# Kernel tuning notes

Hardware: AMD Instinct MI355X
Metric: run time of the kernel (lower is better)

## Reference

```python
import jax, jax.numpy as jnp
import numpy as np

N = 50000   # nodes
E = 800000  # edges
G = 64      # graphs in batch
H1, D1 = 2, 64   # gat1: 2 heads x 64
D2 = 32          # gat2: 1 head x 32
IN = 1
EPS = 1e-5


def _gat(h, src, dst, W, al, ar, Wres, bias, Hh, D):
    # DGL GATConv (eval mode): project, per-edge attention, edge softmax over dst, scatter-sum, residual + bias
    feat = (h @ W).reshape(N, Hh, D)                     # [N,H,D]
    el = jnp.sum(feat * al, axis=-1)                     # [N,H]
    er = jnp.sum(feat * ar, axis=-1)                     # [N,H]
    e = jax.nn.leaky_relu(el[src] + er[dst], 0.2)        # [E,H]
    m = jax.ops.segment_max(e, dst, num_segments=N)      # [N,H] (stable softmax)
    a = jnp.exp(e - m[dst])
    s = jax.ops.segment_sum(a, dst, num_segments=N)
    alpha = a / s[dst]                                   # [E,H]
    msg = feat[src] * alpha[:, :, None]                  # [E,H,D]
    rst = jax.ops.segment_sum(msg, dst, num_segments=N)  # [N,H,D]
    res = (h @ Wres).reshape(N, Hh, D)
    return rst + res + bias.reshape(1, Hh, D)


def _bn(x, gamma, beta, mean, var):
    return (x - mean) * jax.lax.rsqrt(var + EPS) * gamma + beta


def setup_inputs() -> dict:
    key = jax.random.key(0)
    ks = jax.random.split(key, 32)
    rn = lambda i, shape: jax.random.normal(ks[i], shape, jnp.float32) * 0.1
    inp = {
        'feat': jax.random.normal(ks[0], (N, IN), jnp.float32),
        'W1': rn(1, (IN, H1 * D1)), 'al1': rn(2, (H1, D1)), 'ar1': rn(3, (H1, D1)),
        'res1': rn(4, (IN, H1 * D1)), 'b1': rn(5, (H1 * D1,)),
        'g1_gamma': jnp.ones((H1 * D1,), jnp.float32), 'g1_beta': jnp.zeros((H1 * D1,), jnp.float32),
        'g1_mean': rn(6, (H1 * D1,)), 'g1_var': jax.random.uniform(ks[7], (H1 * D1,), jnp.float32) + 0.5,
        'W2': rn(8, (H1 * D1, D2)), 'al2': rn(9, (1, D2)), 'ar2': rn(10, (1, D2)),
        'res2': rn(11, (H1 * D1, D2)), 'b2': rn(12, (D2,)),
        'g2_gamma': jnp.ones((D2,), jnp.float32), 'g2_beta': jnp.zeros((D2,), jnp.float32),
        'g2_mean': rn(13, (D2,)), 'g2_var': jax.random.uniform(ks[14], (D2,), jnp.float32) + 0.5,
        'Wd1': rn(15, (D2, H1 * D1)), 'bd1': rn(16, (H1 * D1,)),
        'gd_gamma': jnp.ones((H1 * D1,), jnp.float32), 'gd_beta': jnp.zeros((H1 * D1,), jnp.float32),
        'gd_mean': rn(17, (H1 * D1,)), 'gd_var': jax.random.uniform(ks[18], (H1 * D1,), jnp.float32) + 0.5,
        'Wd2': rn(19, (H1 * D1, IN)), 'bd2': rn(20, (IN,)),
        'src': jax.random.randint(ks[21], (E,), 0, N, jnp.int32),
        'dst': jax.random.randint(ks[22], (E,), 0, N, jnp.int32),
        'graph_ids': jnp.sort(jax.random.randint(ks[23], (N,), 0, G, jnp.int32)),
    }
    return inp


def reference(feat, W1, al1, ar1, res1, b1, g1_gamma, g1_beta, g1_mean, g1_var,
              W2, al2, ar2, res2, b2, g2_gamma, g2_beta, g2_mean, g2_var,
              Wd1, bd1, gd_gamma, gd_beta, gd_mean, gd_var, Wd2, bd2,
              src, dst, graph_ids):
    h = _gat(feat, src, dst, W1, al1, ar1, res1, b1, H1, D1)   # [N,2,64]
    h = h.reshape(N, H1 * D1)
    h = jax.nn.relu(_bn(h, g1_gamma, g1_beta, g1_mean, g1_var))
    h = _gat(h, src, dst, W2, al2, ar2, res2, b2, 1, D2)       # [N,1,32]
    h = h.reshape(N, D2)
    h = jax.nn.relu(_bn(h, g2_gamma, g2_beta, g2_mean, g2_var))
    # dgl.mean_nodes over batched graphs
    counts = jax.ops.segment_sum(jnp.ones((N,), h.dtype), graph_ids, num_segments=G)
    graph_rep = jax.ops.segment_sum(h, graph_ids, num_segments=G) / jnp.maximum(counts, 1.0)[:, None]
    # decoder: Linear -> BN -> ReLU -> Linear (dropout off in eval)
    d = jax.nn.relu(_bn(h @ Wd1 + bd1, gd_gamma, gd_beta, gd_mean, gd_var))
    reconstruction = d @ Wd2 + bd2
    return graph_rep, reconstruction
```

## Files before the change

### kernel.cpp

```cpp
#include <hip/hip_runtime.h>
#include <hip/hip_bf16.h>

#define NN 50000
#define NE 800000
#define NG 64
#define C1 128
#define D2 32
#define CAP 32
#define BN_EPS 1e-5f

#define CST_A   0
#define CST_B   2
#define CST_P   4
#define CST_Q   132
#define CST_R   260
#define CST_SC2 388
#define CST_RC2 420
#define CST_SD  452
#define CST_RD  580
#define CST_N   1024

#define UO_DEG   0
#define UO_OVFC  50000
#define ZERO_UNITS 50004
#define UO_FLAG  50004
#define UO_CST   50008
#define UO_ESRC2 51040
#define UO_OVF   851040
#define UO_FCAN  2451040
#define UO_F2    2501040
#define UO_RS2   3301040
#define UO_EL2   4901040
#define UO_ER2   4951040
#define UO_END   5001040

__device__ __forceinline__ float lrelu(float x) { return fmaxf(x, 0.2f * x); }
__device__ __forceinline__ float bu2f(unsigned int u) {
    union { unsigned int i; float f; } v; v.i = (u & 0xFFFFu) << 16; return v.f;
}
__device__ __forceinline__ unsigned short f2bu(float f) {
    union { float f; unsigned int i; } v; v.f = f;
    unsigned int r = v.i + 0x7FFFu + ((v.i >> 16) & 1u);
    return (unsigned short)(r >> 16);
}
__device__ __forceinline__ float pk_lo(unsigned int w) {
    union { unsigned int i; float f; } v; v.i = w << 16; return v.f;
}
__device__ __forceinline__ float pk_hi(unsigned int w) {
    union { unsigned int i; float f; } v; v.i = w & 0xFFFF0000u; return v.f;
}
__device__ __forceinline__ float ldw(const void* p, int i, int bf) {
    return bf ? bu2f(((const unsigned short*)p)[i]) : ((const float*)p)[i];
}
__device__ __forceinline__ int sniff64(const unsigned int* fw, int l) {
    int cnt = 0;
    for (int j = l; j < 256; j += 64) {
        unsigned int b = (fw[j] >> 8) & 0x7Fu;
        cnt += (b >= 0x3Au && b <= 0x41u) ? 1 : 0;
    }
#pragma unroll
    for (int m = 32; m >= 1; m >>= 1) cnt += __shfl_xor(cnt, m);
    return (cnt > 128) ? 1 : 0;
}

__global__ void k_prep(const void* __restrict__ feat, const int* __restrict__ dst,
                       const int* __restrict__ src,
                       float* __restrict__ fcan, int* __restrict__ deg,
                       unsigned short* __restrict__ esrc2,
                       int2* __restrict__ ovf, int* __restrict__ ovfc,
                       const void* W1, const void* al1, const void* ar1,
                       const void* res1, const void* b1,
                       const void* g1g, const void* g1b, const void* g1m, const void* g1v,
                       const void* b2v, const void* g2g, const void* g2b,
                       const void* g2m, const void* g2v,
                       const void* bd1, const void* gdg, const void* gdb,
                       const void* gdm, const void* gdv,
                       int* __restrict__ flag, float* __restrict__ cst) {
    __shared__ int sBf;
    int t = threadIdx.x;
    if (t < 64) {
        int bf = sniff64((const unsigned int*)feat, t);
        if (t == 0) sBf = bf;
    }
    __syncthreads();
    int bf = sBf;

    if (blockIdx.x == 0) {
        if (t == 0) *flag = bf;
        if (t < 128) {
            if (t < 2) {
                float a = 0.0f, b = 0.0f;
                for (int d = 0; d < 64; ++d) {
                    float w = ldw(W1, t * 64 + d, bf);
                    a += w * ldw(al1, t * 64 + d, bf);
                    b += w * ldw(ar1, t * 64 + d, bf);
                }
                cst[CST_A + t] = a;
                cst[CST_B + t] = b;
            }
            {
                float sc = rsqrtf(ldw(g1v, t, bf) + BN_EPS) * ldw(g1g, t, bf);
                cst[CST_P + t] = ldw(W1, t, bf) * sc;
                cst[CST_Q + t] = ldw(res1, t, bf) * sc;
                cst[CST_R + t] = (ldw(b1, t, bf) - ldw(g1m, t, bf)) * sc + ldw(g1b, t, bf);
            }
            if (t < D2) {
                float sc = rsqrtf(ldw(g2v, t, bf) + BN_EPS) * ldw(g2g, t, bf);
                cst[CST_SC2 + t] = sc;
                cst[CST_RC2 + t] = (ldw(b2v, t, bf) - ldw(g2m, t, bf)) * sc + ldw(g2b, t, bf);
            }
            {
                float sc = rsqrtf(ldw(gdv, t, bf) + BN_EPS) * ldw(gdg, t, bf);
                cst[CST_SD + t] = sc;
                cst[CST_RD + t] = (ldw(bd1, t, bf) - ldw(gdm, t, bf)) * sc + ldw(gdb, t, bf);
            }
        }
    }

    int k = blockIdx.x * blockDim.x + t;
    if (k < NN) fcan[k] = ldw(feat, k, bf);
    if (k < NE) {
        int d = dst[k];
        int slot = atomicAdd(&deg[d], 1);
        if (slot < CAP) {
            esrc2[d * CAP + slot] = (unsigned short)src[k];
        } else {
            int p = atomicAdd(ovfc, 1);
            ovf[p] = make_int2(d, src[k]);
        }
    }
}

__global__ __launch_bounds__(256) void k_layer1(
        const float* __restrict__ fcan, const void* W2, const void* res2,
        const void* al2, const void* ar2,
        const int* __restrict__ flag, const float* __restrict__ cst,
        const int* __restrict__ deg, const unsigned short* __restrict__ esrc2,
        const int2* __restrict__ ovf, const int* __restrict__ ovfc,
        unsigned short* __restrict__ F2, float* __restrict__ RS2,
        float* __restrict__ EL2, float* __restrict__ ER2) {
    __shared__ unsigned int sW2pk[32 * 66];
    __shared__ unsigned int sR2pk[32 * 66];
    __shared__ unsigned int sH1pk[32 * 66];
    __shared__ float sP[C1], sQ[C1], sR[C1];
    __shared__ float sAl[D2], sAr[D2];
    int t = threadIdx.x;
    int bf = *flag;
    for (int u = t; u < 2048; u += 256) {
        int cw = u >> 5, l2 = u & 31;
        unsigned int wlo = (unsigned int)f2bu(ldw(W2, cw * D2 + l2, bf));
        unsigned int whi = (unsigned int)f2bu(ldw(W2, (cw + 64) * D2 + l2, bf));
        sW2pk[l2 * 66 + cw] = wlo | (whi << 16);
        unsigned int rlo = (unsigned int)f2bu(ldw(res2, cw * D2 + l2, bf));
        unsigned int rhi = (unsigned int)f2bu(ldw(res2, (cw + 64) * D2 + l2, bf));
        sR2pk[l2 * 66 + cw] = rlo | (rhi << 16);
    }
    if (t < C1) { sP[t] = cst[CST_P + t]; sQ[t] = cst[CST_Q + t]; sR[t] = cst[CST_R + t]; }
    if (t < D2) { sAl[t] = ldw(al2, t, bf); sAr[t] = ldw(ar2, t, bf); }
    __syncthreads();

    int l = t & 31;
    int g = t >> 5;
    int base = blockIdx.x * 32;
    float A0 = cst[CST_A + 0], A1 = cst[CST_A + 1];
    float B0 = cst[CST_B + 0], B1 = cst[CST_B + 1];

    int dcap[4], draw[4];
    float fiK[4];
#pragma unroll
    for (int k = 0; k < 4; ++k) {
        int i = base + g * 4 + k;
        if (i < NN) {
            draw[k] = deg[i];
            dcap[k] = draw[k] < CAP ? draw[k] : CAP;
            fiK[k] = fcan[i];
        } else { draw[k] = 0; dcap[k] = 0; fiK[k] = 0.0f; }
    }
    float S0[4], S1[4], N0[4], N1[4];
#pragma unroll
    for (int k = 0; k < 4; ++k) { S0[k] = S1[k] = N0[k] = N1[k] = 0.0f; }
    int sA[4];
#pragma unroll
    for (int k = 0; k < 4; ++k)
        sA[k] = (l < dcap[k]) ? (int)esrc2[(base + g * 4 + k) * CAP + l] : 0;
    float fA[4];
#pragma unroll
    for (int k = 0; k < 4; ++k) fA[k] = fcan[sA[k]];
#pragma unroll
    for (int k = 0; k < 4; ++k) {
        if (l < dcap[k]) {
            float w0 = __expf(lrelu(A0 * fA[k] + B0 * fiK[k]));
            float w1 = __expf(lrelu(A1 * fA[k] + B1 * fiK[k]));
            S0[k] += w0; N0[k] += w0 * fA[k];
            S1[k] += w1; N1[k] += w1 * fA[k];
        }
    }
#pragma unroll
    for (int k = 0; k < 4; ++k) {
        if (draw[k] > CAP) {
            int i = base + g * 4 + k;
            int novf = *ovfc;
            for (int p = l; p < novf; p += 32) {
                int2 o = ovf[p];
                if (o.x == i) {
                    float fs = fcan[o.y];
                    float w0 = __expf(lrelu(A0 * fs + B0 * fiK[k]));
                    float w1 = __expf(lrelu(A1 * fs + B1 * fiK[k]));
                    S0[k] += w0; N0[k] += w0 * fs;
                    S1[k] += w1; N1[k] += w1 * fs;
                }
            }
        }
    }
#pragma unroll
    for (int m = 16; m >= 1; m >>= 1) {
#pragma unroll
        for (int k = 0; k < 4; ++k) {
            S0[k] += __shfl_xor(S0[k], m); N0[k] += __shfl_xor(N0[k], m);
            S1[k] += __shfl_xor(S1[k], m); N1[k] += __shfl_xor(N1[k], m);
        }
    }
#pragma unroll
    for (int k = 0; k < 4; ++k) {
        int slot = g * 4 + k;
        float T0 = S0[k] > 0.0f ? N0[k] / S0[k] : 0.0f;
        float T1 = S1[k] > 0.0f ? N1[k] / S1[k] : 0.0f;
        float h0  = fmaxf(sP[l]      * T0 + sQ[l]      * fiK[k] + sR[l],      0.0f);
        float h1v = fmaxf(sP[l + 32] * T0 + sQ[l + 32] * fiK[k] + sR[l + 32], 0.0f);
        float h2v = fmaxf(sP[l + 64] * T1 + sQ[l + 64] * fiK[k] + sR[l + 64], 0.0f);
        float h3v = fmaxf(sP[l + 96] * T1 + sQ[l + 96] * fiK[k] + sR[l + 96], 0.0f);
        sH1pk[slot * 66 + l]      = (unsigned int)f2bu(h0)  | ((unsigned int)f2bu(h2v) << 16);
        sH1pk[slot * 66 + l + 32] = (unsigned int)f2bu(h1v) | ((unsigned int)f2bu(h3v) << 16);
    }
    __syncthreads();

    int w = t >> 6;
    int half = (t >> 5) & 1;
    int nb0 = w * 8 + half * 4;
    float aF[4] = {0.f, 0.f, 0.f, 0.f}, aR[4] = {0.f, 0.f, 0.f, 0.f};
    for (int cw = 0; cw < 64; cw += 2) {
        uint2 wq = *(const uint2*)&sW2pk[l * 66 + cw];
        uint2 rq = *(const uint2*)&sR2pk[l * 66 + cw];
        float w_a = pk_lo(wq.x), w_b = pk_hi(wq.x), w_c = pk_lo(wq.y), w_d = pk_hi(wq.y);
        float r_a = pk_lo(rq.x), r_b = pk_hi(rq.x), r_c = pk_lo(rq.y), r_d = pk_hi(rq.y);
#pragma unroll
        for (int n = 0; n < 4; ++n) {
            uint2 hq = *(const uint2*)&sH1pk[(nb0 + n) * 66 + cw];
            float h_a = pk_lo(hq.x), h_b = pk_hi(hq.x), h_c = pk_lo(hq.y), h_d = pk_hi(hq.y);
            aF[n] = fmaf(h_a, w_a, fmaf(h_b, w_b, fmaf(h_c, w_c, fmaf(h_d, w_d, aF[n]))));
            aR[n] = fmaf(h_a, r_a, fmaf(h_b, r_b, fmaf(h_c, r_c, fmaf(h_d, r_d, aR[n]))));
        }
    }
#pragma unroll
    for (int n = 0; n < 4; ++n) {
        int i = base + nb0 + n;
        if (i < NN) {
            float elp = aF[n] * sAl[l], erp = aF[n] * sAr[l];
#pragma unroll
            for (int m = 16; m >= 1; m >>= 1) {
                elp += __shfl_xor(elp, m);
                erp += __shfl_xor(erp, m);
            }
            if (l == 0) { EL2[i] = elp; ER2[i] = erp; }
            F2[(size_t)i * D2 + l]  = f2bu(aF[n]);
            RS2[(size_t)i * D2 + l] = aR[n];
        }
    }
}

__global__ __launch_bounds__(256) void k_final(
        const void* Wd1, const void* Wd2, const void* bd2,
        const int* __restrict__ flag, const float* __restrict__ cst,
        const int* __restrict__ deg, const unsigned short* __restrict__ esrc2,
        const int2* __restrict__ ovf, const int* __restrict__ ovfc,
        const unsigned short* __restrict__ F2, float* __restrict__ RS2,
        const float* __restrict__ EL2, const float* __restrict__ ER2,
        float* __restrict__ out) {
    __shared__ float sWd1[C1 * D2];
    __shared__ float sWd2[C1];
    __shared__ float sSd[C1], sRd[C1];
    __shared__ float sSc2[D2], sRc2[D2];
    __shared__ float sH2[8 * D2];
    int t = threadIdx.x;
    int bf = *flag;
    for (int u = t; u < C1 * D2; u += 256) sWd1[u] = ldw(Wd1, u, bf);
    for (int u = t; u < C1; u += 256) {
        sWd2[u] = ldw(Wd2, u, bf);
        sSd[u] = cst[CST_SD + u]; sRd[u] = cst[CST_RD + u];
    }
    if (t < D2) { sSc2[t] = cst[CST_SC2 + t]; sRc2[t] = cst[CST_RC2 + t]; }
    __syncthreads();

    int i = (blockIdx.x * 256 + t) >> 5;
    int l = t & 31;
    int nb = t >> 5;

    float eri = ER2[i];
    int dr = deg[i];
    int dcap = dr < CAP ? dr : CAP;
    const unsigned short* row = &esrc2[i * CAP];
    float aF0 = 0.f, aF1 = 0.f, aF2 = 0.f, aF3 = 0.f, aF4 = 0.f, aF5 = 0.f, aF6 = 0.f, aF7 = 0.f;
    float S0 = 0.f, S1 = 0.f, S2 = 0.f, S3 = 0.f, S4 = 0.f, S5 = 0.f, S6 = 0.f, S7 = 0.f;
    int j = 0;
    for (; j + 7 < dcap; j += 8) {
        uint4 qq = *(const uint4*)&row[j];
        int s0 = qq.x & 0xFFFF, s1 = qq.x >> 16;
        int s2 = qq.y & 0xFFFF, s3 = qq.y >> 16;
        int s4 = qq.z & 0xFFFF, s5 = qq.z >> 16;
        int s6 = qq.w & 0xFFFF, s7 = qq.w >> 16;
        float w0 = __expf(lrelu(EL2[s0] + eri));
        float w1 = __expf(lrelu(EL2[s1] + eri));
        float w2 = __expf(lrelu(EL2[s2] + eri));
        float w3 = __expf(lrelu(EL2[s3] + eri));
        float w4 = __expf(lrelu(EL2[s4] + eri));
        float w5 = __expf(lrelu(EL2[s5] + eri));
        float w6 = __expf(lrelu(EL2[s6] + eri));
        float w7 = __expf(lrelu(EL2[s7] + eri));
        float v0 = bu2f(F2[(size_t)s0 * D2 + l]);
        float v1 = bu2f(F2[(size_t)s1 * D2 + l]);
        float v2 = bu2f(F2[(size_t)s2 * D2 + l]);
        float v3 = bu2f(F2[(size_t)s3 * D2 + l]);
        float v4 = bu2f(F2[(size_t)s4 * D2 + l]);
        float v5 = bu2f(F2[(size_t)s5 * D2 + l]);
        float v6 = bu2f(F2[(size_t)s6 * D2 + l]);
        float v7 = bu2f(F2[(size_t)s7 * D2 + l]);
        S0 += w0; S1 += w1; S2 += w2; S3 += w3;
        S4 += w4; S5 += w5; S6 += w6; S7 += w7;
        aF0 = fmaf(w0, v0, aF0); aF1 = fmaf(w1, v1, aF1);
        aF2 = fmaf(w2, v2, aF2); aF3 = fmaf(w3, v3, aF3);
        aF4 = fmaf(w4, v4, aF4); aF5 = fmaf(w5, v5, aF5);
        aF6 = fmaf(w6, v6, aF6); aF7 = fmaf(w7, v7, aF7);
    }
    for (; j + 3 < dcap; j += 4) {
        ushort4 q = *(const ushort4*)&row[j];
        int sA = q.x, sB = q.y, sC = q.z, sD = q.w;
        float wA = __expf(lrelu(EL2[sA] + eri));
        float wB = __expf(lrelu(EL2[sB] + eri));
        float wC = __expf(lrelu(EL2[sC] + eri));
        float wD = __expf(lrelu(EL2[sD] + eri));
        float vA = bu2f(F2[(size_t)sA * D2 + l]);
        float vB = bu2f(F2[(size_t)sB * D2 + l]);
        float vC = bu2f(F2[(size_t)sC * D2 + l]);
        float vD = bu2f(F2[(size_t)sD * D2 + l]);
        S0 += wA; S1 += wB; S2 += wC; S3 += wD;
        aF0 = fmaf(wA, vA, aF0); aF1 = fmaf(wB, vB, aF1);
        aF2 = fmaf(wC, vC, aF2); aF3 = fmaf(wD, vD, aF3);
    }
    for (; j < dcap; ++j) {
        int sA = (int)row[j];
        float wA = __expf(lrelu(EL2[sA] + eri));
        S0 += wA;
        aF0 = fmaf(wA, bu2f(F2[(size_t)sA * D2 + l]), aF0);
    }
    if (dr > CAP) {
        int novf = *ovfc;
        for (int p = 0; p < novf; ++p) {
            int2 o = ovf[p];
            if (o.x == i) {
                float wA = __expf(lrelu(EL2[o.y] + eri));
                S0 += wA;
                aF0 = fmaf(wA, bu2f(F2[(size_t)o.y * D2 + l]), aF0);
            }
        }
    }
    float S = ((S0 + S1) + (S2 + S3)) + ((S4 + S5) + (S6 + S7));
    float aF = ((aF0 + aF1) + (aF2 + aF3)) + ((aF4 + aF5) + (aF6 + aF7));
    float inv = S > 0.0f ? 1.0f / S : 0.0f;

    float h2 = fmaxf((aF * inv + RS2[(size_t)i * D2 + l]) * sSc2[l] + sRc2[l], 0.0f);
    RS2[(size_t)i * D2 + l] = h2;

    sH2[nb * D2 + l] = h2;
    float ac0 = 0.0f, ac1 = 0.0f, ac2 = 0.0f, ac3 = 0.0f;
#pragma unroll
    for (int d = 0; d < D2; ++d) {
        float h = sH2[nb * D2 + d];
        const float* wr = &sWd1[d * C1 + l];
        ac0 = fmaf(h, wr[0],  ac0);
        ac1 = fmaf(h, wr[32], ac1);
        ac2 = fmaf(h, wr[64], ac2);
        ac3 = fmaf(h, wr[96], ac3);
    }
    float rec = fmaxf(ac0 * sSd[l]      + sRd[l],      0.0f) * sWd2[l]
              + fmaxf(ac1 * sSd[l + 32] + sRd[l + 32], 0.0f) * sWd2[l + 32]
              + fmaxf(ac2 * sSd[l + 64] + sRd[l + 64], 0.0f) * sWd2[l + 64]
              + fmaxf(ac3 * sSd[l + 96] + sRd[l + 96], 0.0f) * sWd2[l + 96];
#pragma unroll
    for (int m = 16; m >= 1; m >>= 1) rec += __shfl_xor(rec, m);
    if (l == 0) out[NG * D2 + i] = rec + ldw(bd2, 0, bf);
}

__global__ __launch_bounds__(256) void k_pool2(const int* __restrict__ gid,
                                               const float* __restrict__ H2,
                                               float* __restrict__ out) {
    __shared__ int sLo, sHi;
    __shared__ float sAcc[32 * 32];
    int g = blockIdx.x;
    int t = threadIdx.x;
    if (t == 0) {
        int lo = 0, hi = NN;
        while (lo < hi) { int m = (lo + hi) >> 1; if (gid[m] < g) lo = m + 1; else hi = m; }
        sLo = lo;
        lo = 0; hi = NN;
        while (lo < hi) { int m = (lo + hi) >> 1; if (gid[m] < g + 1) lo = m + 1; else hi = m; }
        sHi = lo;
    }
    __syncthreads();
    int lo = sLo, hi = sHi;
    int q = t & 7;
    int row = t >> 3;
    float4 acc = make_float4(0.f, 0.f, 0.f, 0.f);
    for (int i = lo + row; i < hi; i += 32) {
        float4 v = ((const float4*)&H2[(size_t)i * D2])[q];
        acc.x += v.x; acc.y += v.y; acc.z += v.z; acc.w += v.w;
    }
    *(float4*)&sAcc[row * 32 + 4 * q] = acc;
    __syncthreads();
    if (t < 32) {
        float a = 0.0f;
        for (int r = 0; r < 32; ++r) a += sAcc[r * 32 + t];
        float c = (float)(hi - lo);
        out[g * D2 + t] = a / fmaxf(c, 1.0f);
    }
}

extern "C" void kernel_launch(void* const* d_in, const int* in_sizes, int n_in,
                              void* d_out, int out_size, void* d_ws, size_t ws_size,
                              hipStream_t stream) {
    const void* feat = d_in[0];
    const void* W1 = d_in[1];  const void* al1 = d_in[2];  const void* ar1 = d_in[3];
    const void* res1 = d_in[4]; const void* b1 = d_in[5];
    const void* g1g = d_in[6]; const void* g1b = d_in[7];
    const void* g1m = d_in[8]; const void* g1v = d_in[9];
    const void* W2 = d_in[10]; const void* al2 = d_in[11]; const void* ar2 = d_in[12];
    const void* res2 = d_in[13]; const void* b2v = d_in[14];
    const void* g2g = d_in[15]; const void* g2b = d_in[16];
    const void* g2m = d_in[17]; const void* g2v = d_in[18];
    const void* Wd1 = d_in[19]; const void* bd1 = d_in[20];
    const void* gdg = d_in[21]; const void* gdb = d_in[22];
    const void* gdm = d_in[23]; const void* gdv = d_in[24];
    const void* Wd2 = d_in[25]; const void* bd2 = d_in[26];
    const int* src = (const int*)d_in[27];
    const int* dst = (const int*)d_in[28];
    const int* gid = (const int*)d_in[29];

    unsigned int* wsu = (unsigned int*)d_ws;
    int* deg    = (int*)(wsu + UO_DEG);
    int* ovfc   = (int*)(wsu + UO_OVFC);
    int* flag   = (int*)(wsu + UO_FLAG);
    float* cst  = (float*)(wsu + UO_CST);
    unsigned short* esrc2 = (unsigned short*)(wsu + UO_ESRC2);
    int2* ovf   = (int2*)(wsu + UO_OVF);
    float* fcan = (float*)(wsu + UO_FCAN);
    unsigned short* F2 = (unsigned short*)(wsu + UO_F2);
    float* RS2  = (float*)(wsu + UO_RS2);
    float* EL2  = (float*)(wsu + UO_EL2);
    float* ER2  = (float*)(wsu + UO_ER2);

    hipMemsetAsync(d_ws, 0, (size_t)ZERO_UNITS * 4, stream);

    k_prep<<<(NE + 255) / 256, 256, 0, stream>>>(feat, dst, src, fcan, deg,
                                                 esrc2, ovf, ovfc,
                                                 W1, al1, ar1, res1, b1,
                                                 g1g, g1b, g1m, g1v,
                                                 b2v, g2g, g2b, g2m, g2v,
                                                 bd1, gdg, gdb, gdm, gdv,
                                                 flag, cst);

    k_layer1<<<(NN + 31) / 32, 256, 0, stream>>>(fcan, W2, res2, al2, ar2, flag, cst,
                                                 deg, esrc2, ovf, ovfc,
                                                 F2, RS2, EL2, ER2);

    k_final<<<(NN * 32) / 256, 256, 0, stream>>>(Wd1, Wd2, bd2, flag, cst,
                                                 deg, esrc2, ovf, ovfc,
                                                 F2, RS2, EL2, ER2,
                                                 (float*)d_out);

    k_pool2<<<NG, 256, 0, stream>>>(gid, RS2, (float*)d_out);
}
```

Baseline: 259.5 us.

## Partition edge bucketing by destination range and pad degree counters

The edge bucketing in k_prep now runs 8 blocks per 2048-edge chunk, each handling only destinations in one of 8 node ranges (blockIdx & 7). The intent is to keep atomics and esrc2 writes for a given node range inside fewer blocks, which is likely meant to line up with XCD-local L2 on the MI355X. Degree counters are also padded to one per 64-byte slot (stride 16 ints) to cut atomic contention from false sharing. In exchange every block reads all dst values in its chunk, so dst traffic rises 8x, and the memset grows from about 200 KB to 3.2 MB.

```diff
diff --git a/kernel.cpp b/kernel.cpp
--- a/kernel.cpp
+++ b/kernel.cpp
@@ -7,6 +7,8 @@
 #define C1 128
 #define D2 32
 #define CAP 32
+#define RNG 6250
+#define NCH 391
 #define BN_EPS 1e-5f
 
 #define CST_A   0
@@ -20,19 +22,19 @@
 #define CST_RD  580
 #define CST_N   1024
 
-#define UO_DEG   0
-#define UO_OVFC  50000
-#define ZERO_UNITS 50004
-#define UO_FLAG  50004
-#define UO_CST   50008
-#define UO_ESRC2 51040
-#define UO_OVF   851040
-#define UO_FCAN  2451040
-#define UO_F2    2501040
-#define UO_RS2   3301040
-#define UO_EL2   4901040
-#define UO_ER2   4951040
-#define UO_END   5001040
+#define UO_DEGP  0
+#define UO_OVFC  800000
+#define ZERO_UNITS 800004
+#define UO_FLAG  800004
+#define UO_CST   800008
+#define UO_ESRC2 801040
+#define UO_OVF   1601040
+#define UO_FCAN  3201040
+#define UO_F2    3251040
+#define UO_RS2   4051040
+#define UO_EL2   5651040
+#define UO_ER2   5701040
+#define UO_END   5751040
 
 __device__ __forceinline__ float lrelu(float x) { return fmaxf(x, 0.2f * x); }
 __device__ __forceinline__ float bu2f(unsigned int u) {
@@ -65,7 +67,7 @@
 
 __global__ void k_prep(const void* __restrict__ feat, const int* __restrict__ dst,
                        const int* __restrict__ src,
-                       float* __restrict__ fcan, int* __restrict__ deg,
+                       float* __restrict__ fcan, int* __restrict__ degp,
                        unsigned short* __restrict__ esrc2,
                        int2* __restrict__ ovf, int* __restrict__ ovfc,
                        const void* W1, const void* al1, const void* ar1,
@@ -84,6 +86,8 @@
     }
     __syncthreads();
     int bf = sBf;
+    int r = blockIdx.x & 7;
+    int c = blockIdx.x >> 3;
 
     if (blockIdx.x == 0) {
         if (t == 0) *flag = bf;
@@ -117,17 +121,23 @@
         }
     }
 
-    int k = blockIdx.x * blockDim.x + t;
-    if (k < NN) fcan[k] = ldw(feat, k, bf);
-    if (k < NE) {
-        int d = dst[k];
-        int slot = atomicAdd(&deg[d], 1);
-        if (slot < CAP) {
-            esrc2[d * CAP + slot] = (unsigned short)src[k];
-        } else {
-            int p = atomicAdd(ovfc, 1);
-            ovf[p] = make_int2(d, src[k]);
-        }
+    int lo = r * RNG, hi = lo + RNG;
+#pragma unroll
+    for (int j = 0; j < 8; ++j) {
+        int k = c * 2048 + j * 256 + t;
+        if (k < NE) {
+            int d = dst[k];
+            if (d >= lo && d < hi) {
+                int slot = atomicAdd(&degp[d << 4], 1);
+                if (slot < CAP) {
+                    esrc2[d * CAP + slot] = (unsigned short)src[k];
+                } else {
+                    int p = atomicAdd(ovfc, 1);
+                    ovf[p] = make_int2(d, src[k]);
+                }
+            }
+        }
+        if (r == 0 && k < NN) fcan[k] = ldw(feat, k, bf);
     }
 }
 
@@ -135,7 +145,7 @@
         const float* __restrict__ fcan, const void* W2, const void* res2,
         const void* al2, const void* ar2,
         const int* __restrict__ flag, const float* __restrict__ cst,
-        const int* __restrict__ deg, const unsigned short* __restrict__ esrc2,
+        const int* __restrict__ degp, const unsigned short* __restrict__ esrc2,
         const int2* __restrict__ ovf, const int* __restrict__ ovfc,
         unsigned short* __restrict__ F2, float* __restrict__ RS2,
         float* __restrict__ EL2, float* __restrict__ ER2) {
@@ -171,7 +181,7 @@
     for (int k = 0; k < 4; ++k) {
         int i = base + g * 4 + k;
         if (i < NN) {
-            draw[k] = deg[i];
+            draw[k] = degp[i << 4];
             dcap[k] = draw[k] < CAP ? draw[k] : CAP;
             fiK[k] = fcan[i];
         } else { draw[k] = 0; dcap[k] = 0; fiK[k] = 0.0f; }
@@ -271,7 +281,7 @@
 __global__ __launch_bounds__(256) void k_final(
         const void* Wd1, const void* Wd2, const void* bd2,
         const int* __restrict__ flag, const float* __restrict__ cst,
-        const int* __restrict__ deg, const unsigned short* __restrict__ esrc2,
+        const int* __restrict__ degp, const unsigned short* __restrict__ esrc2,
         const int2* __restrict__ ovf, const int* __restrict__ ovfc,
         const unsigned short* __restrict__ F2, float* __restrict__ RS2,
         const float* __restrict__ EL2, const float* __restrict__ ER2,
@@ -296,7 +306,7 @@
     int nb = t >> 5;
 
     float eri = ER2[i];
-    int dr = deg[i];
+    int dr = degp[i << 4];
     int dcap = dr < CAP ? dr : CAP;
     const unsigned short* row = &esrc2[i * CAP];
     float aF0 = 0.f, aF1 = 0.f, aF2 = 0.f, aF3 = 0.f, aF4 = 0.f, aF5 = 0.f, aF6 = 0.f, aF7 = 0.f;
@@ -445,7 +455,7 @@
     const int* gid = (const int*)d_in[29];
 
     unsigned int* wsu = (unsigned int*)d_ws;
-    int* deg    = (int*)(wsu + UO_DEG);
+    int* degp   = (int*)(wsu + UO_DEGP);
     int* ovfc   = (int*)(wsu + UO_OVFC);
     int* flag   = (int*)(wsu + UO_FLAG);
     float* cst  = (float*)(wsu + UO_CST);
@@ -459,20 +469,20 @@
 
     hipMemsetAsync(d_ws, 0, (size_t)ZERO_UNITS * 4, stream);
 
-    k_prep<<<(NE + 255) / 256, 256, 0, stream>>>(feat, dst, src, fcan, deg,
-                                                 esrc2, ovf, ovfc,
-                                                 W1, al1, ar1, res1, b1,
-                                                 g1g, g1b, g1m, g1v,
-                                                 b2v, g2g, g2b, g2m, g2v,
-                                                 bd1, gdg, gdb, gdm, gdv,
-                                                 flag, cst);
+    k_prep<<<NCH * 8, 256, 0, stream>>>(feat, dst, src, fcan, degp,
+                                        esrc2, ovf, ovfc,
+                                        W1, al1, ar1, res1, b1,
+                                        g1g, g1b, g1m, g1v,
+                                        b2v, g2g, g2b, g2m, g2v,
+                                        bd1, gdg, gdb, gdm, gdv,
+                                        flag, cst);
 
     k_layer1<<<(NN + 31) / 32, 256, 0, stream>>>(fcan, W2, res2, al2, ar2, flag, cst,
-                                                 deg, esrc2, ovf, ovfc,
+                                                 degp, esrc2, ovf, ovfc,
                                                  F2, RS2, EL2, ER2);
 
     k_final<<<(NN * 32) / 256, 256, 0, stream>>>(Wd1, Wd2, bd2, flag, cst,
-                                                 deg, esrc2, ovf, ovfc,
+                                                 degp, esrc2, ovf, ovfc,
                                                  F2, RS2, EL2, ER2,
                                                  (float*)d_out);
 
```

New measurement: 257.1 us. About the same (-0.9%).
